# Optimization experiments

Measured on AMD Instinct MI355X. Metric: run time of the kernel, lower is better.

Reference implementation:

```python
import jax, jax.numpy as jnp
import numpy as np

B, S, W, H = 16, 512, 8, 768  # batch, seq_len, max_span width, hidden_dim


def setup_inputs() -> dict:
    key = jax.random.key(0)
    ks = jax.random.split(key, 6)
    return {
        "hidden": jax.random.normal(ks[0], (B, S, H), jnp.float32),
        "term_weight": jax.random.normal(ks[1], (H,), jnp.float32),
        "w1": jax.random.normal(ks[2], (H, 64), jnp.float32) * 0.02,
        "b1": jnp.zeros((64,), jnp.float32),
        "w2": jax.random.normal(ks[3], (64, 1), jnp.float32) * 0.05,
        "b2": jnp.zeros((1,), jnp.float32),
        "w_score": jax.random.normal(ks[4], (H, 2), jnp.float32) * 0.02,
        "b_score": jnp.zeros((2,), jnp.float32),
    }


def reference(hidden, term_weight, w1, b1, w2, b2, w_score, b_score):
    # TermAttention token logits: MLP(hidden * termWeight) depends only on the
    # token, not the span, so compute once per token instead of per span.
    ah = hidden * term_weight                                  # [B,S,H]
    tok_logit = (jax.nn.relu(ah @ w1 + b1) @ w2 + b2)[..., 0]  # [B,S]

    starts = jnp.arange(S)
    offs = jnp.arange(W)
    # candidate span (start s, width w) covers tokens s .. min(s+w, S-1)
    tok_idx = jnp.minimum(starts[:, None] + offs[None, :], S - 1)      # [S,W]
    span_len = jnp.minimum(offs[None, :] + 1, S - starts[:, None])    # [S,W]

    Lg = tok_logit[:, tok_idx]   # [B,S,W] gathered per-position logits
    Hg = hidden[:, tok_idx]      # [B,S,W,H] gathered per-position hiddens

    # pos_mask[s,w,j] = position j is inside span (s, width w)
    pos_mask = offs[None, None, :] < span_len[:, :, None]              # [S,W,W]
    logits = jnp.where(pos_mask[None], Lg[:, :, None, :], -jnp.inf)   # [B,S,W,W]
    attn = jax.nn.softmax(logits, axis=-1)                             # [B,S,W,W]

    # span embedding = attention-weighted sum of span token hiddens
    emb = jnp.einsum('bswj,bsjh->bswh', attn, Hg)                      # [B,S,W,H]
    scores = emb @ w_score + b_score                                   # [B,S,W,2]
    return scores
```

## Files before the change

kernel.cpp:

```cpp
#include <hip/hip_runtime.h>

#define S_LEN 512
#define H_DIM 768
#define BS_TOK 8192
#define NCOLS 80
#define KSPLIT 4
#define KSEG 192
#define KPAD 200
#define CPAD 68

typedef __attribute__((ext_vector_type(8))) short short8v;
typedef __attribute__((ext_vector_type(4))) short short4v;
typedef __attribute__((ext_vector_type(4))) float f32x4;

__device__ __forceinline__ short f2bf(float f) {
  union { float f; unsigned u; } x; x.f = f;
  unsigned r = x.u + 0x7fffu + ((x.u >> 16) & 1u);
  return (short)(r >> 16);
}


__global__ __launch_bounds__(256) void k1f(const float* __restrict__ hidden,
                                           const float* __restrict__ tw,
                                           const float* __restrict__ w1,
                                           const float* __restrict__ wsc,
                                           float* __restrict__ part) {
  __shared__ short bs[NCOLS * KPAD];
  const int tid  = threadIdx.x;
  const int bid  = blockIdx.x;
  const int tile = bid >> 2;
  const int kseg = bid & 3;
  const int k0   = kseg * KSEG;

#pragma unroll
  for (int i = 0; i < 12; ++i) {
    int e = tid + 256 * i;
    int koff = e >> 4, c4 = e & 15;
    int k = k0 + koff;
    float twk = tw[k];
    float4 w = *reinterpret_cast<const float4*>(w1 + (size_t)k * 64 + c4 * 4);
    bs[(c4 * 4 + 0) * KPAD + koff] = f2bf(w.x * twk);
    bs[(c4 * 4 + 1) * KPAD + koff] = f2bf(w.y * twk);
    bs[(c4 * 4 + 2) * KPAD + koff] = f2bf(w.z * twk);
    bs[(c4 * 4 + 3) * KPAD + koff] = f2bf(w.w * twk);
  }
#pragma unroll
  for (int i = 0; i < 2; ++i) {
    int e = tid + 256 * i;
    if (e < 2 * KSEG) {
      int koff = e >> 1, c = e & 1;
      bs[(64 + c) * KPAD + koff] = f2bf(wsc[(size_t)(k0 + koff) * 2 + c]);
    }
  }
  if (tid < KSEG) {
#pragma unroll
    for (int c = 66; c < 80; ++c) bs[c * KPAD + tid] = 0;
  }
  __syncthreads();

  const int w    = tid >> 6;
  const int lane = tid & 63;
  const int ci   = lane & 15;
  const int g    = lane >> 4;
  const int kg   = g * 8;
  const int r0   = tile * 64 + w * 16;

  f32x4 acc[5];
#pragma unroll
  for (int nt = 0; nt < 5; ++nt) acc[nt] = (f32x4){0.f, 0.f, 0.f, 0.f};

  const float* aptr = hidden + (size_t)(r0 + ci) * H_DIM + k0 + kg;
#pragma unroll
  for (int ks = 0; ks < KSEG; ks += 32) {
    float4 a0 = *reinterpret_cast<const float4*>(aptr + ks);
    float4 a1 = *reinterpret_cast<const float4*>(aptr + ks + 4);
    short8v av;
    av[0] = f2bf(a0.x); av[1] = f2bf(a0.y); av[2] = f2bf(a0.z); av[3] = f2bf(a0.w);
    av[4] = f2bf(a1.x); av[5] = f2bf(a1.y); av[6] = f2bf(a1.z); av[7] = f2bf(a1.w);
#pragma unroll
    for (int nt = 0; nt < 5; ++nt) {
      short8v bb = *reinterpret_cast<const short8v*>(&bs[(nt * 16 + ci) * KPAD + ks + kg]);
      acc[nt] = __builtin_amdgcn_mfma_f32_16x16x32_bf16(av, bb, acc[nt], 0, 0, 0);
    }
  }

  float* pr = part + ((size_t)kseg * BS_TOK + r0) * CPAD;
#pragma unroll
  for (int j = 0; j < 4; ++j) {
    int r = 4 * g + j;
#pragma unroll
    for (int nt = 0; nt < 4; ++nt)
      pr[r * CPAD + nt * 16 + ci] = acc[nt][j];
    if (ci < 2) pr[r * CPAD + 64 + ci] = acc[4][j];
  }
}

__global__ __launch_bounds__(256) void k2f(const float* __restrict__ part,
                                           const float* __restrict__ b1,
                                           const float* __restrict__ w2,
                                           const float* __restrict__ b2,
                                           float* __restrict__ logit,
                                           float* __restrict__ pbuf) {
  const int tid  = threadIdx.x;
  const int w    = tid >> 6;
  const int lane = tid & 63;
  const int ci   = lane & 15;
  const int tt   = blockIdx.x * 16 + w * 4 + (lane >> 4);

  f32x4 s = (f32x4){0.f, 0.f, 0.f, 0.f};
#pragma unroll
  for (int seg = 0; seg < KSPLIT; ++seg) {
    const float4 v = *reinterpret_cast<const float4*>(
        part + ((size_t)seg * BS_TOK + tt) * CPAD + 4 * ci);
    s[0] += v.x; s[1] += v.y; s[2] += v.z; s[3] += v.w;
  }
  const float4 bb = *reinterpret_cast<const float4*>(b1 + 4 * ci);
  const float4 ww = *reinterpret_cast<const float4*>(w2 + 4 * ci);
  float r = fmaxf(s[0] + bb.x, 0.f) * ww.x + fmaxf(s[1] + bb.y, 0.f) * ww.y +
            fmaxf(s[2] + bb.z, 0.f) * ww.z + fmaxf(s[3] + bb.w, 0.f) * ww.w;
#pragma unroll
  for (int msk = 1; msk < 16; msk <<= 1) r += __shfl_xor(r, msk, 64);

  if (ci < 2) {
    float pv = 0.f;
#pragma unroll
    for (int seg = 0; seg < KSPLIT; ++seg)
      pv += part[((size_t)seg * BS_TOK + tt) * CPAD + 64 + ci];
    if (ci == 0) logit[tt] = r + b2[0];
    pbuf[2 * tt + ci] = pv;
  }
}

__global__ __launch_bounds__(256) void k3(const float* __restrict__ logit,
                                          const float* __restrict__ pbuf,
                                          const float* __restrict__ bsc,
                                          float* __restrict__ out) {
  int t = blockIdx.x * 256 + threadIdx.x;
  int s = t & (S_LEN - 1);
  int nmax = min(8, S_LEN - s);
  float bs0 = bsc[0], bs1 = bsc[1];
  float m = logit[t];
  float d = 1.f;
  float n0 = pbuf[2 * t], n1 = pbuf[2 * t + 1];
  float o[16];
  o[0] = n0 + bs0; o[1] = n1 + bs1;
#pragma unroll
  for (int j = 1; j < 8; ++j) {
    if (j < nmax) {
      float L  = logit[t + j];
      float nm = fmaxf(m, L);
      float sc = __expf(m - nm);
      float e  = __expf(L - nm);
      d  = d  * sc + e;
      n0 = n0 * sc + e * pbuf[2 * (t + j)];
      n1 = n1 * sc + e * pbuf[2 * (t + j) + 1];
      m = nm;
    }
    float inv = 1.f / d;
    o[2 * j]     = n0 * inv + bs0;
    o[2 * j + 1] = n1 * inv + bs1;
  }
  float4* op = reinterpret_cast<float4*>(out + (size_t)t * 16);
#pragma unroll
  for (int i = 0; i < 4; ++i) op[i] = *reinterpret_cast<float4*>(&o[4 * i]);
}


__global__ __launch_bounds__(256) void kprep(const float* __restrict__ tw,
                                             const float* __restrict__ w1,
                                             const float* __restrict__ wsc,
                                             short* __restrict__ wcat) {
  int i = blockIdx.x * 256 + threadIdx.x;
  if (i >= NCOLS * H_DIM) return;
  int c = i / H_DIM, k = i - c * H_DIM;
  float v = 0.f;
  if (c < 64)       v = tw[k] * w1[k * 64 + c];
  else if (c == 64) v = wsc[k * 2 + 0];
  else if (c == 65) v = wsc[k * 2 + 1];
  wcat[i] = f2bf(v);
}

__global__ __launch_bounds__(256) void k1s(const float* __restrict__ hidden,
                                           const short* __restrict__ wcat,
                                           const float* __restrict__ b1,
                                           const float* __restrict__ w2,
                                           const float* __restrict__ b2,
                                           float* __restrict__ logit,
                                           float* __restrict__ pbuf) {
  __shared__ short as[64 * 72];
  __shared__ short bss[NCOLS * 72];
  const int tid  = threadIdx.x;
  const int t0   = blockIdx.x * 64;
  const int w    = tid >> 6;
  const int lane = tid & 63;
  const int ci   = lane & 15;
  const int kg   = (lane >> 4) * 8;
  const int arow = w * 16 + ci;

  f32x4 acc[5];
#pragma unroll
  for (int nt = 0; nt < 5; ++nt) acc[nt] = (f32x4){0.f, 0.f, 0.f, 0.f};

  for (int cc = 0; cc < H_DIM / 64; ++cc) {
    const int k0 = cc * 64;
    __syncthreads();
#pragma unroll
    for (int i = 0; i < 4; ++i) {
      int f = tid + 256 * i;
      int r = f >> 4, c4 = f & 15;
      const float4 v = *reinterpret_cast<const float4*>(
          hidden + (size_t)(t0 + r) * H_DIM + k0 + c4 * 4);
      short4v bv;
      bv[0] = f2bf(v.x); bv[1] = f2bf(v.y); bv[2] = f2bf(v.z); bv[3] = f2bf(v.w);
      *reinterpret_cast<short4v*>(&as[r * 72 + c4 * 4]) = bv;
    }
    for (int i = tid; i < NCOLS * 8; i += 256) {
      int r = i >> 3, c8 = i & 7;
      short8v v = *reinterpret_cast<const short8v*>(wcat + r * H_DIM + k0 + c8 * 8);
      *reinterpret_cast<short8v*>(&bss[r * 72 + c8 * 8]) = v;
    }
    __syncthreads();
#pragma unroll
    for (int ks = 0; ks < 64; ks += 32) {
      short8v a = *reinterpret_cast<const short8v*>(&as[arow * 72 + ks + kg]);
#pragma unroll
      for (int nt = 0; nt < 5; ++nt) {
        short8v bb = *reinterpret_cast<const short8v*>(&bss[(nt * 16 + ci) * 72 + ks + kg]);
        acc[nt] = __builtin_amdgcn_mfma_f32_16x16x32_bf16(a, bb, acc[nt], 0, 0, 0);
      }
    }
  }

  const int g = lane >> 4;
  float lg[4];
#pragma unroll
  for (int j = 0; j < 4; ++j) {
    float sacc = 0.f;
#pragma unroll
    for (int nt = 0; nt < 4; ++nt) {
      int c = nt * 16 + ci;
      float z = acc[nt][j] + b1[c];
      z = fmaxf(z, 0.f);
      sacc += z * w2[c];
    }
#pragma unroll
    for (int msk = 1; msk < 16; msk <<= 1) sacc += __shfl_xor(sacc, msk, 64);
    lg[j] = sacc;
  }
  const float b2v = b2[0];
#pragma unroll
  for (int j = 0; j < 4; ++j) {
    int rg = t0 + w * 16 + 4 * g + j;
    if (ci == 0) {
      logit[rg] = lg[j] + b2v;
      pbuf[rg * 2 + 0] = acc[4][j];
    } else if (ci == 1) {
      pbuf[rg * 2 + 1] = acc[4][j];
    }
  }
}


extern "C" void kernel_launch(void* const* d_in, const int* in_sizes, int n_in,
                              void* d_out, int out_size, void* d_ws, size_t ws_size,
                              hipStream_t stream) {
  const float* hidden = (const float*)d_in[0];
  const float* tw     = (const float*)d_in[1];
  const float* w1     = (const float*)d_in[2];
  const float* b1     = (const float*)d_in[3];
  const float* w2     = (const float*)d_in[4];
  const float* b2     = (const float*)d_in[5];
  const float* wsc    = (const float*)d_in[6];
  const float* bsc    = (const float*)d_in[7];
  float* out = (float*)d_out;
  char* ws = (char*)d_ws;

  const size_t part_bytes = (size_t)KSPLIT * BS_TOK * CPAD * 4;
  const size_t need_fast  = part_bytes + 32768 + 65536;

  if (ws_size >= need_fast) {
    float* part  = (float*)ws;
    float* logit = (float*)(ws + part_bytes);
    float* pbuf  = (float*)(ws + part_bytes + 32768);
    k1f<<<(BS_TOK / 64) * KSPLIT, 256, 0, stream>>>(hidden, tw, w1, wsc, part);
    k2f<<<BS_TOK / 16, 256, 0, stream>>>(part, b1, w2, b2, logit, pbuf);
    k3 <<<BS_TOK / 256, 256, 0, stream>>>(logit, pbuf, bsc, out);
  } else {
    short* wcat  = (short*)ws;
    float* logit = (float*)(ws + 131072);
    float* pbuf  = (float*)(ws + 131072 + 32768);
    kprep<<<(NCOLS * H_DIM + 255) / 256, 256, 0, stream>>>(tw, w1, wsc, wcat);
    k1s<<<BS_TOK / 64, 256, 0, stream>>>(hidden, wcat, b1, w2, b2, logit, pbuf);
    k3<<<BS_TOK / 256, 256, 0, stream>>>(logit, pbuf, bsc, out);
  }
}
```

Measured before the change: 21.19 us.

## Fuse split-K reduction with span softmax, store partials in fp16, halve GEMM tiles

Merges the split-K reduction kernel and the span-attention kernel into one. Each block recomputes logits for its token window plus a 7-token halo in shared memory, which removes one launch and the logit/pbuf round trip through global memory. The partial-sum buffer is stored as fp16 instead of fp32 to cut write and read traffic. The first GEMM kernel uses 32-row tiles with 128 threads so more blocks are launched. The costs are some redundant halo work, reduced precision in the partial sums, and the shared-weight staging being repeated across twice as many blocks.

```diff
diff --git a/kernel.cpp b/kernel.cpp
--- a/kernel.cpp
+++ b/kernel.cpp
@@ -7,11 +7,14 @@
 #define KSPLIT 4
 #define KSEG 192
 #define KPAD 200
-#define CPAD 68
+#define PSTRIDE 72
+#define BM 32
+#define TOKB 32
 
 typedef __attribute__((ext_vector_type(8))) short short8v;
 typedef __attribute__((ext_vector_type(4))) short short4v;
 typedef __attribute__((ext_vector_type(4))) float f32x4;
+typedef __attribute__((ext_vector_type(4))) _Float16 h4;
 
 __device__ __forceinline__ short f2bf(float f) {
   union { float f; unsigned u; } x; x.f = f;
@@ -19,12 +22,11 @@
   return (short)(r >> 16);
 }
 
-
-__global__ __launch_bounds__(256) void k1f(const float* __restrict__ hidden,
+__global__ __launch_bounds__(128) void k1f(const float* __restrict__ hidden,
                                            const float* __restrict__ tw,
                                            const float* __restrict__ w1,
                                            const float* __restrict__ wsc,
-                                           float* __restrict__ part) {
+                                           _Float16* __restrict__ part) {
   __shared__ short bs[NCOLS * KPAD];
   const int tid  = threadIdx.x;
   const int bid  = blockIdx.x;
@@ -33,8 +35,8 @@
   const int k0   = kseg * KSEG;
 
 #pragma unroll
-  for (int i = 0; i < 12; ++i) {
-    int e = tid + 256 * i;
+  for (int i = 0; i < 24; ++i) {
+    int e = tid + 128 * i;
     int koff = e >> 4, c4 = e & 15;
     int k = k0 + koff;
     float twk = tw[k];
@@ -45,16 +47,16 @@
     bs[(c4 * 4 + 3) * KPAD + koff] = f2bf(w.w * twk);
   }
 #pragma unroll
-  for (int i = 0; i < 2; ++i) {
-    int e = tid + 256 * i;
+  for (int i = 0; i < 3; ++i) {
+    int e = tid + 128 * i;
     if (e < 2 * KSEG) {
       int koff = e >> 1, c = e & 1;
       bs[(64 + c) * KPAD + koff] = f2bf(wsc[(size_t)(k0 + koff) * 2 + c]);
     }
   }
-  if (tid < KSEG) {
-#pragma unroll
-    for (int c = 66; c < 80; ++c) bs[c * KPAD + tid] = 0;
+  for (int i = tid; i < 14 * KSEG; i += 128) {
+    int c = 66 + i / KSEG, koff = i - (c - 66) * KSEG;
+    bs[c * KPAD + koff] = 0;
   }
   __syncthreads();
 
@@ -63,7 +65,7 @@
   const int ci   = lane & 15;
   const int g    = lane >> 4;
   const int kg   = g * 8;
-  const int r0   = tile * 64 + w * 16;
+  const int r0   = tile * BM + w * 16;
 
   f32x4 acc[5];
 #pragma unroll
@@ -84,85 +86,93 @@
     }
   }
 
-  float* pr = part + ((size_t)kseg * BS_TOK + r0) * CPAD;
+  _Float16* pr = part + ((size_t)kseg * BS_TOK + r0) * PSTRIDE;
 #pragma unroll
   for (int j = 0; j < 4; ++j) {
     int r = 4 * g + j;
 #pragma unroll
     for (int nt = 0; nt < 4; ++nt)
-      pr[r * CPAD + nt * 16 + ci] = acc[nt][j];
-    if (ci < 2) pr[r * CPAD + 64 + ci] = acc[4][j];
-  }
-}
-
-__global__ __launch_bounds__(256) void k2f(const float* __restrict__ part,
-                                           const float* __restrict__ b1,
-                                           const float* __restrict__ w2,
-                                           const float* __restrict__ b2,
-                                           float* __restrict__ logit,
-                                           float* __restrict__ pbuf) {
+      pr[r * PSTRIDE + nt * 16 + ci] = (_Float16)acc[nt][j];
+    if (ci < 2) pr[r * PSTRIDE + 64 + ci] = (_Float16)acc[4][j];
+  }
+}
+
+__global__ __launch_bounds__(256) void kB(const _Float16* __restrict__ part,
+                                          const float* __restrict__ b1,
+                                          const float* __restrict__ w2,
+                                          const float* __restrict__ b2,
+                                          const float* __restrict__ bsc,
+                                          float* __restrict__ out) {
+  __shared__ float lp[TOKB + 8][4];
   const int tid  = threadIdx.x;
+  const int t0   = blockIdx.x * TOKB;
   const int w    = tid >> 6;
   const int lane = tid & 63;
   const int ci   = lane & 15;
-  const int tt   = blockIdx.x * 16 + w * 4 + (lane >> 4);
-
-  f32x4 s = (f32x4){0.f, 0.f, 0.f, 0.f};
-#pragma unroll
-  for (int seg = 0; seg < KSPLIT; ++seg) {
-    const float4 v = *reinterpret_cast<const float4*>(
-        part + ((size_t)seg * BS_TOK + tt) * CPAD + 4 * ci);
-    s[0] += v.x; s[1] += v.y; s[2] += v.z; s[3] += v.w;
-  }
-  const float4 bb = *reinterpret_cast<const float4*>(b1 + 4 * ci);
-  const float4 ww = *reinterpret_cast<const float4*>(w2 + 4 * ci);
-  float r = fmaxf(s[0] + bb.x, 0.f) * ww.x + fmaxf(s[1] + bb.y, 0.f) * ww.y +
-            fmaxf(s[2] + bb.z, 0.f) * ww.z + fmaxf(s[3] + bb.w, 0.f) * ww.w;
-#pragma unroll
-  for (int msk = 1; msk < 16; msk <<= 1) r += __shfl_xor(r, msk, 64);
-
-  if (ci < 2) {
-    float pv = 0.f;
-#pragma unroll
-    for (int seg = 0; seg < KSPLIT; ++seg)
-      pv += part[((size_t)seg * BS_TOK + tt) * CPAD + 64 + ci];
-    if (ci == 0) logit[tt] = r + b2[0];
-    pbuf[2 * tt + ci] = pv;
-  }
-}
-
-__global__ __launch_bounds__(256) void k3(const float* __restrict__ logit,
-                                          const float* __restrict__ pbuf,
-                                          const float* __restrict__ bsc,
-                                          float* __restrict__ out) {
-  int t = blockIdx.x * 256 + threadIdx.x;
-  int s = t & (S_LEN - 1);
-  int nmax = min(8, S_LEN - s);
-  float bs0 = bsc[0], bs1 = bsc[1];
-  float m = logit[t];
-  float d = 1.f;
-  float n0 = pbuf[2 * t], n1 = pbuf[2 * t + 1];
-  float o[16];
-  o[0] = n0 + bs0; o[1] = n1 + bs1;
-#pragma unroll
-  for (int j = 1; j < 8; ++j) {
-    if (j < nmax) {
-      float L  = logit[t + j];
-      float nm = fmaxf(m, L);
-      float sc = __expf(m - nm);
-      float e  = __expf(L - nm);
-      d  = d  * sc + e;
-      n0 = n0 * sc + e * pbuf[2 * (t + j)];
-      n1 = n1 * sc + e * pbuf[2 * (t + j) + 1];
-      m = nm;
-    }
-    float inv = 1.f / d;
-    o[2 * j]     = n0 * inv + bs0;
-    o[2 * j + 1] = n1 * inv + bs1;
-  }
-  float4* op = reinterpret_cast<float4*>(out + (size_t)t * 16);
-#pragma unroll
-  for (int i = 0; i < 4; ++i) op[i] = *reinterpret_cast<float4*>(&o[4 * i]);
+  const int grp  = lane >> 4;
+  const int base = w * 4 + grp;
+
+#pragma unroll
+  for (int pass = 0; pass < 3; ++pass) {
+    int slot = pass * 16 + base;
+    if (slot < TOKB + 7) {
+      int tt = min(t0 + slot, BS_TOK - 1);
+      f32x4 s = (f32x4){0.f, 0.f, 0.f, 0.f};
+#pragma unroll
+      for (int seg = 0; seg < KSPLIT; ++seg) {
+        h4 v = *reinterpret_cast<const h4*>(
+            part + ((size_t)seg * BS_TOK + tt) * PSTRIDE + 4 * ci);
+        s[0] += (float)v[0]; s[1] += (float)v[1];
+        s[2] += (float)v[2]; s[3] += (float)v[3];
+      }
+      const float4 bb = *reinterpret_cast<const float4*>(b1 + 4 * ci);
+      const float4 ww = *reinterpret_cast<const float4*>(w2 + 4 * ci);
+      float r = fmaxf(s[0] + bb.x, 0.f) * ww.x + fmaxf(s[1] + bb.y, 0.f) * ww.y +
+                fmaxf(s[2] + bb.z, 0.f) * ww.z + fmaxf(s[3] + bb.w, 0.f) * ww.w;
+#pragma unroll
+      for (int msk = 1; msk < 16; msk <<= 1) r += __shfl_xor(r, msk, 64);
+      if (ci == 0) lp[slot][0] = r + b2[0];
+      if (ci < 2) {
+        float pv = 0.f;
+#pragma unroll
+        for (int seg = 0; seg < KSPLIT; ++seg)
+          pv += (float)part[((size_t)seg * BS_TOK + tt) * PSTRIDE + 64 + ci];
+        lp[slot][1 + ci] = pv;
+      }
+    }
+  }
+  __syncthreads();
+
+  if (tid < TOKB) {
+    int t = t0 + tid;
+    int s_ = t & (S_LEN - 1);
+    int nmax = min(8, S_LEN - s_);
+    float bs0 = bsc[0], bs1 = bsc[1];
+    float m = lp[tid][0];
+    float d = 1.f;
+    float n0 = lp[tid][1], n1 = lp[tid][2];
+    float o[16];
+    o[0] = n0 + bs0; o[1] = n1 + bs1;
+#pragma unroll
+    for (int j = 1; j < 8; ++j) {
+      if (j < nmax) {
+        float L  = lp[tid + j][0];
+        float nm = fmaxf(m, L);
+        float sc = __expf(m - nm);
+        float e  = __expf(L - nm);
+        d  = d  * sc + e;
+        n0 = n0 * sc + e * lp[tid + j][1];
+        n1 = n1 * sc + e * lp[tid + j][2];
+        m = nm;
+      }
+      float inv = 1.f / d;
+      o[2 * j]     = n0 * inv + bs0;
+      o[2 * j + 1] = n1 * inv + bs1;
+    }
+    float4* op = reinterpret_cast<float4*>(out + (size_t)t * 16);
+#pragma unroll
+    for (int i = 0; i < 4; ++i) op[i] = *reinterpret_cast<float4*>(&o[4 * i]);
+  }
 }
 
 
@@ -260,6 +270,40 @@
   }
 }
 
+__global__ __launch_bounds__(256) void k3g(const float* __restrict__ logit,
+                                           const float* __restrict__ pbuf,
+                                           const float* __restrict__ bsc,
+                                           float* __restrict__ out) {
+  int t = blockIdx.x * 256 + threadIdx.x;
+  int s = t & (S_LEN - 1);
+  int nmax = min(8, S_LEN - s);
+  float bs0 = bsc[0], bs1 = bsc[1];
+  float m = logit[t];
+  float d = 1.f;
+  float n0 = pbuf[2 * t], n1 = pbuf[2 * t + 1];
+  float o[16];
+  o[0] = n0 + bs0; o[1] = n1 + bs1;
+#pragma unroll
+  for (int j = 1; j < 8; ++j) {
+    if (j < nmax) {
+      float L  = logit[t + j];
+      float nm = fmaxf(m, L);
+      float sc = __expf(m - nm);
+      float e  = __expf(L - nm);
+      d  = d  * sc + e;
+      n0 = n0 * sc + e * pbuf[2 * (t + j)];
+      n1 = n1 * sc + e * pbuf[2 * (t + j) + 1];
+      m = nm;
+    }
+    float inv = 1.f / d;
+    o[2 * j]     = n0 * inv + bs0;
+    o[2 * j + 1] = n1 * inv + bs1;
+  }
+  float4* op = reinterpret_cast<float4*>(out + (size_t)t * 16);
+#pragma unroll
+  for (int i = 0; i < 4; ++i) op[i] = *reinterpret_cast<float4*>(&o[4 * i]);
+}
+
 
 extern "C" void kernel_launch(void* const* d_in, const int* in_sizes, int n_in,
                               void* d_out, int out_size, void* d_ws, size_t ws_size,
@@ -275,22 +319,18 @@
   float* out = (float*)d_out;
   char* ws = (char*)d_ws;
 
-  const size_t part_bytes = (size_t)KSPLIT * BS_TOK * CPAD * 4;
-  const size_t need_fast  = part_bytes + 32768 + 65536;
-
-  if (ws_size >= need_fast) {
-    float* part  = (float*)ws;
-    float* logit = (float*)(ws + part_bytes);
-    float* pbuf  = (float*)(ws + part_bytes + 32768);
-    k1f<<<(BS_TOK / 64) * KSPLIT, 256, 0, stream>>>(hidden, tw, w1, wsc, part);
-    k2f<<<BS_TOK / 16, 256, 0, stream>>>(part, b1, w2, b2, logit, pbuf);
-    k3 <<<BS_TOK / 256, 256, 0, stream>>>(logit, pbuf, bsc, out);
+  const size_t part_bytes = (size_t)KSPLIT * BS_TOK * PSTRIDE * 2;
+
+  if (ws_size >= part_bytes) {
+    _Float16* part = (_Float16*)ws;
+    k1f<<<(BS_TOK / BM) * KSPLIT, 128, 0, stream>>>(hidden, tw, w1, wsc, part);
+    kB <<<BS_TOK / TOKB, 256, 0, stream>>>(part, b1, w2, b2, bsc, out);
   } else {
     short* wcat  = (short*)ws;
     float* logit = (float*)(ws + 131072);
     float* pbuf  = (float*)(ws + 131072 + 32768);
     kprep<<<(NCOLS * H_DIM + 255) / 256, 256, 0, stream>>>(tw, w1, wsc, wcat);
     k1s<<<BS_TOK / 64, 256, 0, stream>>>(hidden, wcat, b1, w2, b2, logit, pbuf);
-    k3<<<BS_TOK / 256, 256, 0, stream>>>(logit, pbuf, bsc, out);
-  }
-}
+    k3g<<<BS_TOK / 256, 256, 0, stream>>>(logit, pbuf, bsc, out);
+  }
+}
```

New measurement: 22.97 us. 8.4% more time.
